# Optimization experiments

Hardware: AMD Instinct MI355X
Metric: run time of the kernel (lower is better)

Reference implementation:

```python
import jax, jax.numpy as jnp
import numpy as np

B, N, U = 8, 2048, 256
BN_EPS = 1e-3  # keras BatchNormalization default epsilon
ADJ_DENSITY = 0.008  # ~16 neighbors per node on average


def setup_inputs() -> dict:
    key = jax.random.key(0)
    ks = jax.random.split(key, 16)
    s = 0.05  # weight scale ('random_normal' init is small-stddev in keras)
    x = jax.random.normal(ks[0], (B, N, U), jnp.float32)
    # sparse binary adjacency stored dense (per-sample SpMM pattern)
    adj = (jax.random.uniform(ks[1], (B, N, N)) < ADJ_DENSITY).astype(jnp.float32)
    nodal_mask = jnp.ones((B, N), jnp.float32)
    return {
        'x': x, 'adj': adj, 'nodal_mask': nodal_mask,
        'W_lin': jax.random.normal(ks[2], (U, U)) * s, 'b_lin': jnp.zeros((U,)),
        'Wq_mp': jax.random.normal(ks[3], (3, U, U)) * s, 'bq_mp': jnp.zeros((3, U)),
        'Wk_mp': jax.random.normal(ks[4], (3, U, U)) * s, 'bk_mp': jnp.zeros((3, U)),
        'Wv_mp': jax.random.normal(ks[5], (3, U, U)) * s, 'bv_mp': jnp.zeros((3, U)),
        'Wk_att': jax.random.normal(ks[6], (U, U)) * s,
        'Wv_att': jax.random.normal(ks[7], (U, U)) * s,
        'Wq_att': jax.random.normal(ks[8], (U, U)) * s,
        'Wo_att': jax.random.normal(ks[9], (U, U)) * s,
        'bn_gamma': jnp.ones((U,)), 'bn_beta': jnp.zeros((U,)),
        'bn_mean': jnp.zeros((U,)), 'bn_var': jnp.ones((U,)),
        'W_proj': jax.random.normal(ks[10], (U, U)) * s, 'b_proj': jnp.zeros((U,)),
        'W_res': jax.random.normal(ks[11], (U, U)) * s, 'b_res': jnp.zeros((U,)),
    }


def _dympn(x, adj, Ws, bs, mask):
    # 3 message-passing layers, each applied K_l=2 times (inference value)
    for i in range(3):
        for _ in range(2):
            xn = jnp.einsum('bmn,bnd->bmd', adj, x)  # batched SpMM (graph_conv mode)
            x = jax.nn.silu(jnp.einsum('bmd,de->bme', xn, Ws[i]) + bs[i])
    return x * mask[:, :, None]


def reference(x, adj, nodal_mask, W_lin, b_lin, Wq_mp, bq_mp, Wk_mp, bk_mp,
              Wv_mp, bv_mp, Wk_att, Wv_att, Wq_att, Wo_att,
              bn_gamma, bn_beta, bn_mean, bn_var, W_proj, b_proj, W_res, b_res):
    initial_x = x
    adj = jax.lax.stop_gradient(adj)
    h = jnp.einsum('bnd,de->bne', x, W_lin) + b_lin
    q = _dympn(h, adj, Wq_mp, bq_mp, nodal_mask)
    k = _dympn(h, adj, Wk_mp, bk_mp, nodal_mask)
    v = _dympn(h, adj, Wv_mp, bv_mp, nodal_mask)
    # linear attention
    m = nodal_mask[:, :, None]
    pk = jax.nn.silu(jnp.einsum('bnd,de->bne', k, Wk_att) * m)
    pv = jnp.einsum('bnd,de->bne', v, Wv_att) * m
    pq = jnp.einsum('bnd,de->bne', q, Wq_att)
    kv = jnp.einsum('bnd,bne->bde', pk, pv)       # [B,U,U]
    attn = jnp.einsum('bnd,bde->bne', pq, kv)
    attn = jnp.einsum('bnd,de->bne', attn, Wo_att)
    # batch norm (inference: moving stats) over last axis
    y = attn + initial_x
    y = bn_gamma * (y - bn_mean) * jax.lax.rsqrt(bn_var + BN_EPS) + bn_beta
    out = jax.nn.silu(jnp.einsum('bnd,de->bne', y, W_proj) + b_proj)
    out = out + jnp.einsum('bnd,de->bne', initial_x, W_res) + b_res
    out = out * nodal_mask[:, :, None]
    return out
```

## Files before the change

kernel.cpp:

```cpp
#include <hip/hip_runtime.h>
#include <stdint.h>

#define NB 8
#define NN 2048
#define NU 256
#define CAP 64
#define BNEPS 0.001f
#define GSTR ((size_t)(NN * NU + 256))

typedef __attribute__((ext_vector_type(8))) short short8;
typedef __attribute__((ext_vector_type(4))) float floatx4;
typedef unsigned short u16;
typedef unsigned int u32;

__device__ __forceinline__ float bf2f(u16 u) {
  union { u32 i; float f; } c; c.i = ((u32)u) << 16; return c.f;
}
__device__ __forceinline__ u16 f2bf(float f) {
  union { float f; u32 i; } c; c.f = f;
  return (u16)((c.i + 0x7fffu + ((c.i >> 16) & 1u)) >> 16);
}
__device__ __forceinline__ void splitbf(float a, u16& h, u16& l) {
  h = f2bf(a);
  l = f2bf(a - bf2f(h));
}

enum : unsigned {
  F_BIAS = 2u, F_SILU = 4u, F_MASKPRE = 8u, F_MASKPOST = 16u,
  F_ADDX = 32u, F_BN = 64u, F_ADDT = 128u, F_BPERMAT = 512u,
  F_TPLANES = 1024u, F_OUTHL = 2048u, F_GSTRIDE = 8192u
};

#define TP_MAT 524288
#define TP_LO  4194304
#define MSZ ((size_t)NN * NU)

struct WPtrs { const float* p[16]; };

__global__ __launch_bounds__(256) void prologue_k(
    WPtrs wp, u16* __restrict__ wdst,
    const float* __restrict__ x, u16* __restrict__ xdst, size_t xLo,
    const float* __restrict__ adj, int* __restrict__ cnt, int* __restrict__ idx,
    float* __restrict__ ga, float* __restrict__ gb)
{
  int bid = blockIdx.x;
  int tid = threadIdx.x;
  __shared__ int c0;
  if (bid < 512) {
    int gid = bid * 256 + tid;
    int mat = gid >> 13;
    int rem = gid & 8191;
    int kb = rem >> 10;
    int n = (rem >> 2) & 255;
    int slot = rem & 3;
    int qv = (slot - (n >> 1)) & 3;
    int k0 = kb * 32 + qv * 8;
    const float* W = wp.p[mat];
    u32 oh[4], ol[4];
#pragma unroll
    for (int t2 = 0; t2 < 4; t2++) {
      float f0 = W[(size_t)(k0 + 2 * t2) * 256 + n];
      float f1 = W[(size_t)(k0 + 2 * t2 + 1) * 256 + n];
      u16 h0, l0, h1, l1;
      splitbf(f0, h0, l0);
      splitbf(f1, h1, l1);
      oh[t2] = (u32)h0 | ((u32)h1 << 16);
      ol[t2] = (u32)l0 | ((u32)l1 << 16);
    }
    uint4 qh; qh.x = oh[0]; qh.y = oh[1]; qh.z = oh[2]; qh.w = oh[3];
    uint4 ql; ql.x = ol[0]; ql.y = ol[1]; ql.z = ol[2]; ql.w = ol[3];
    *(uint4*)(wdst + (size_t)gid * 8) = qh;
    *(uint4*)(wdst + 1048576 + (size_t)gid * 8) = ql;
  } else if (bid < 4608) {
    size_t i = ((size_t)(bid - 512) * 256 + tid) * 4;
    float4 v = *(const float4*)(x + i);
    u16 h0, l0, h1, l1, h2, l2, h3, l3;
    splitbf(v.x, h0, l0); splitbf(v.y, h1, l1);
    splitbf(v.z, h2, l2); splitbf(v.w, h3, l3);
    uint2 H; H.x = (u32)h0 | ((u32)h1 << 16); H.y = (u32)h2 | ((u32)h3 << 16);
    uint2 L; L.x = (u32)l0 | ((u32)l1 << 16); L.y = (u32)l2 | ((u32)l3 << 16);
    *(uint2*)(xdst + i) = H;
    *(uint2*)(xdst + xLo + i) = L;
  } else if (bid < 20992) {
    int row = bid - 4608;
    const float* base = adj + (size_t)row * NN;
    if (tid == 0) c0 = 0;
    __syncthreads();
#pragma unroll
    for (int j = 0; j < 8; j++) {
      int n = j * 256 + tid;
      if (base[n] != 0.f) {
        int p = atomicAdd(&c0, 1);
        if (p < CAP) idx[(size_t)row * CAP + p] = n;
      }
    }
    __syncthreads();
    int cc = (c0 < CAP ? c0 : CAP);
    for (int p = cc + tid; p < CAP; p += 256) idx[(size_t)row * CAP + p] = -1;
    if (tid == 0) cnt[row] = cc;
  } else {
    int g = bid - 20992;
    float* base = (g < 24 ? ga : gb) + (size_t)(g % 24) * GSTR;
    base[tid] = 0.f;
  }
}

template <unsigned F>
__device__ __forceinline__ void gemm_epi(
    floatx4 (&acc)[2][2], int b, int bm, int w, int m16, int q,
    const float* __restrict__ bias, const float* __restrict__ mask,
    const float* __restrict__ xf32,
    const float* __restrict__ gma, const float* __restrict__ bta,
    const float* __restrict__ bmu, const float* __restrict__ bvr,
    const float* __restrict__ addt, void* __restrict__ outp, size_t oLo)
{
#pragma unroll
  for (int mt = 0; mt < 2; mt++) {
    if (F & F_TPLANES) {
      u16* oh = (u16*)outp + (size_t)b * TP_MAT;
      u16* ol = oh + TP_LO;
      int gr0 = bm + mt * 16 + q * 4;
#pragma unroll
      for (int nt = 0; nt < 2; nt++) {
        int col = w * 32 + nt * 16 + m16;
        u16 hh[4], ll[4];
#pragma unroll
        for (int r = 0; r < 4; r++) {
          float t2 = acc[mt][nt][r];
          float mv = mask[b * NN + gr0 + r];
          if (F & F_MASKPRE) t2 *= mv;
          if (F & F_SILU) t2 = t2 / (1.f + __expf(-t2));
          if (F & F_MASKPOST) t2 *= mv;
          splitbf(t2, hh[r], ll[r]);
        }
        uint2 H2, L2v;
        H2.x = (u32)hh[0] | ((u32)hh[1] << 16);
        H2.y = (u32)hh[2] | ((u32)hh[3] << 16);
        L2v.x = (u32)ll[0] | ((u32)ll[1] << 16);
        L2v.y = (u32)ll[2] | ((u32)ll[3] << 16);
        *(uint2*)(oh + (size_t)col * 2048 + gr0) = H2;
        *(uint2*)(ol + (size_t)col * 2048 + gr0) = L2v;
      }
    } else {
#pragma unroll
      for (int r = 0; r < 4; r++) {
        int gr = bm + mt * 16 + q * 4 + r;
        float mval = 1.f;
        if (F & (F_MASKPRE | F_MASKPOST)) mval = mask[b * NN + gr];
#pragma unroll
        for (int nt = 0; nt < 2; nt++) {
          int col = w * 32 + nt * 16 + m16;
          float t2 = acc[mt][nt][r];
          if (F & F_BIAS) t2 += bias[col];
          if (F & F_MASKPRE) t2 *= mval;
          if (F & F_SILU) t2 = t2 / (1.f + __expf(-t2));
          if (F & F_ADDX) t2 += xf32[((size_t)b * NN + gr) * NU + col];
          if (F & F_BN) t2 = gma[col] * (t2 - bmu[col]) * rsqrtf(bvr[col] + BNEPS) + bta[col];
          if (F & F_ADDT) t2 += addt[((size_t)b * NN + gr) * NU + col];
          if (F & F_MASKPOST) t2 *= mval;
          size_t o;
          if (F & F_GSTRIDE) o = (size_t)b * GSTR + (size_t)gr * NU + col;
          else o = ((size_t)b * NN + gr) * NU + col;
          if (F & F_OUTHL) {
            u16 h0, l0;
            splitbf(t2, h0, l0);
            ((u16*)outp)[o] = h0;
            ((u16*)outp)[o + oLo] = l0;
          } else {
            ((float*)outp)[o] = t2;
          }
        }
      }
    }
  }
}

#define LDSPAD_U16 28672

template <int NG, unsigned SF, unsigned F0, unsigned F1, unsigned F2, bool DK = false>
__global__ __launch_bounds__(512, 8) void gemm_k(
    const u16* __restrict__ A0, const u16* __restrict__ A1, const u16* __restrict__ A2,
    size_t aLo,
    const u16* __restrict__ W0, const u16* __restrict__ W1, const u16* __restrict__ W2,
    size_t wLo,
    const float* __restrict__ b0, const float* __restrict__ b1, const float* __restrict__ b2,
    const float* __restrict__ mask,
    const float* __restrict__ xf32,
    const float* __restrict__ gma, const float* __restrict__ bta,
    const float* __restrict__ bmu, const float* __restrict__ bvr,
    const float* __restrict__ addt,
    void* __restrict__ o0, void* __restrict__ o1, void* __restrict__ o2,
    size_t oLo,
    const float* __restrict__ gsrc,
    const float* __restrict__ sb0, const float* __restrict__ sb1, const float* __restrict__ sb2,
    const int* __restrict__ ncnt, const int* __restrict__ nidx)
{
  const int tid = threadIdx.x;
  const int id = blockIdx.x;
  const int xcd = id & 7;
  const int t = id >> 3;
  const int chain = (NG == 1) ? 0 : (t >> 6);
  const int xt = (NG == 1) ? t : (t & 63);
  const int b = xcd;
  const int bm = xt * 32;

  __shared__ alignas(16) u16 AB[LDSPAD_U16];
  u16* const Ah = AB;
  u16* const Al = AB + 32 * 264;

  const u16* Wsel = (chain == 0) ? W0 : (chain == 1 ? W1 : W2);
  if (F0 & F_BPERMAT) Wsel = W0 + (size_t)b * 65536;
  const u16* Whi = Wsel;
  const u16* Wlo = Whi + wLo;

  const int lane = tid & 63;
  const int w = tid >> 6;

  if constexpr (SF != 0u) {
    const float* __restrict__ gm = gsrc + (size_t)(chain * 8 + b) * GSTR + 256;
    const float* sb = (chain == 0) ? sb0 : (chain == 1 ? sb1 : sb2);
    const int c = lane * 4;
    float4 bb = *(const float4*)(sb + c);
    const int r0 = w * 4;
    int cnts[4];
    const int* ips[4];
    float4 av[4];
    int rowids[4];
#pragma unroll
    for (int i = 0; i < 4; i++) {
      rowids[i] = b * NN + bm + r0 + i;
      cnts[i] = ncnt[rowids[i]];
      ips[i] = nidx + (size_t)rowids[i] * CAP;
      av[i].x = av[i].y = av[i].z = av[i].w = 0.f;
    }
    int maxc = cnts[0];
    maxc = cnts[1] > maxc ? cnts[1] : maxc;
    maxc = cnts[2] > maxc ? cnts[2] : maxc;
    maxc = cnts[3] > maxc ? cnts[3] : maxc;
    for (int e = 0; e + 4 <= maxc; e += 4) {
#pragma unroll
      for (int i = 0; i < 4; i++) {
        if (e + 4 <= cnts[i]) {
          int4 i4 = *(const int4*)(ips[i] + e);
          float4 v0 = *(const float4*)(gm + ((size_t)i4.x << 8) + c);
          float4 v1 = *(const float4*)(gm + ((size_t)i4.y << 8) + c);
          float4 v2 = *(const float4*)(gm + ((size_t)i4.z << 8) + c);
          float4 v3 = *(const float4*)(gm + ((size_t)i4.w << 8) + c);
          av[i].x += v0.x + v1.x + v2.x + v3.x;
          av[i].y += v0.y + v1.y + v2.y + v3.y;
          av[i].z += v0.z + v1.z + v2.z + v3.z;
          av[i].w += v0.w + v1.w + v2.w + v3.w;
        }
      }
    }
#pragma unroll
    for (int i = 0; i < 4; i++) {
      for (int e = cnts[i] & ~3; e < cnts[i]; e++) {
        float4 v = *(const float4*)(gm + ((size_t)ips[i][e] << 8) + c);
        av[i].x += v.x; av[i].y += v.y; av[i].z += v.z; av[i].w += v.w;
      }
    }
#pragma unroll
    for (int i = 0; i < 4; i++) {
      float ov[4] = {av[i].x + bb.x, av[i].y + bb.y, av[i].z + bb.z, av[i].w + bb.w};
      float mv = (SF & F_MASKPOST) ? mask[rowids[i]] : 1.f;
      u16 hh[4], ll[4];
#pragma unroll
      for (int j = 0; j < 4; j++) {
        float t2 = ov[j];
        if (SF & F_SILU) t2 = t2 / (1.f + __expf(-t2));
        if (SF & F_MASKPOST) t2 *= mv;
        splitbf(t2, hh[j], ll[j]);
      }
      uint2 H; H.x = (u32)hh[0] | ((u32)hh[1] << 16); H.y = (u32)hh[2] | ((u32)hh[3] << 16);
      uint2 L; L.x = (u32)ll[0] | ((u32)ll[1] << 16); L.y = (u32)ll[2] | ((u32)ll[3] << 16);
      *(uint2*)&Ah[(r0 + i) * 264 + c] = H;
      *(uint2*)&Al[(r0 + i) * 264 + c] = L;
    }
  } else {
    const u16* Abase = (chain == 0) ? A0 : (chain == 1 ? A1 : A2);
    const u16* Ahp = Abase + (size_t)b * MSZ;
    const u16* Alp = Ahp + aLo;
    {
      int s = tid;
      int r = s >> 4;
      int c = (s & 15) << 4;
      size_t ao = (size_t)(bm + r) * 256 + c;
      *(uint4*)&Ah[r * 264 + c] = *(const uint4*)(Ahp + ao);
      *(uint4*)&Ah[r * 264 + c + 8] = *(const uint4*)(Ahp + ao + 8);
      *(uint4*)&Al[r * 264 + c] = *(const uint4*)(Alp + ao);
      *(uint4*)&Al[r * 264 + c + 8] = *(const uint4*)(Alp + ao + 8);
    }
  }
  __syncthreads();

  const int m16 = lane & 15;
  const int q = lane >> 4;

  floatx4 acc[2][2];
#pragma unroll
  for (int i = 0; i < 2; i++)
#pragma unroll
    for (int j = 0; j < 2; j++) acc[i][j] = (floatx4){0.f, 0.f, 0.f, 0.f};

#pragma unroll
  for (int kk = 0; kk < 8; kk++) {
    short8 bh[2], bl2[2];
#pragma unroll
    for (int nt = 0; nt < 2; nt++) {
      int n = w * 32 + nt * 16 + m16;
      size_t off = (size_t)kk * 8192 + (size_t)n * 32 + (size_t)(((q + (n >> 1)) & 3) * 8);
      bh[nt] = *(const short8*)(Whi + off);
      bl2[nt] = *(const short8*)(Wlo + off);
    }
#pragma unroll
    for (int mt = 0; mt < 2; mt++) {
      int row = mt * 16 + m16;
      short8 ah = *(const short8*)&Ah[row * 264 + kk * 32 + q * 8];
      short8 al2 = *(const short8*)&Al[row * 264 + kk * 32 + q * 8];
#pragma unroll
      for (int nt = 0; nt < 2; nt++) {
        acc[mt][nt] = __builtin_amdgcn_mfma_f32_16x16x32_bf16(ah, bh[nt], acc[mt][nt], 0, 0, 0);
        acc[mt][nt] = __builtin_amdgcn_mfma_f32_16x16x32_bf16(al2, bh[nt], acc[mt][nt], 0, 0, 0);
        acc[mt][nt] = __builtin_amdgcn_mfma_f32_16x16x32_bf16(ah, bl2[nt], acc[mt][nt], 0, 0, 0);
      }
    }
  }

  if constexpr (DK) {
#pragma unroll
    for (int mt = 0; mt < 2; mt++)
#pragma unroll
      for (int nt = 0; nt < 2; nt++) {
        int col = w * 32 + nt * 16 + m16;
        float bp = b1[col];
#pragma unroll
        for (int r = 0; r < 4; r++) {
          float t2 = acc[mt][nt][r] + bp;
          acc[mt][nt][r] = t2 / (1.f + __expf(-t2));
        }
      }
    __syncthreads();
    {
      const u16* Ahp = A1 + (size_t)b * MSZ;
      const u16* Alp = Ahp + aLo;
      int s = tid;
      int r = s >> 4;
      int c = (s & 15) << 4;
      size_t ao = (size_t)(bm + r) * 256 + c;
      *(uint4*)&Ah[r * 264 + c] = *(const uint4*)(Ahp + ao);
      *(uint4*)&Ah[r * 264 + c + 8] = *(const uint4*)(Ahp + ao + 8);
      *(uint4*)&Al[r * 264 + c] = *(const uint4*)(Alp + ao);
      *(uint4*)&Al[r * 264 + c + 8] = *(const uint4*)(Alp + ao + 8);
    }
    __syncthreads();
    const u16* W1h = W1;
    const u16* W1l = W1 + wLo;
#pragma unroll
    for (int kk = 0; kk < 8; kk++) {
      short8 bh[2], bl2[2];
#pragma unroll
      for (int nt = 0; nt < 2; nt++) {
        int n = w * 32 + nt * 16 + m16;
        size_t off = (size_t)kk * 8192 + (size_t)n * 32 + (size_t)(((q + (n >> 1)) & 3) * 8);
        bh[nt] = *(const short8*)(W1h + off);
        bl2[nt] = *(const short8*)(W1l + off);
      }
#pragma unroll
      for (int mt = 0; mt < 2; mt++) {
        int row = mt * 16 + m16;
        short8 ah = *(const short8*)&Ah[row * 264 + kk * 32 + q * 8];
        short8 al2 = *(const short8*)&Al[row * 264 + kk * 32 + q * 8];
#pragma unroll
        for (int nt = 0; nt < 2; nt++) {
          acc[mt][nt] = __builtin_amdgcn_mfma_f32_16x16x32_bf16(ah, bh[nt], acc[mt][nt], 0, 0, 0);
          acc[mt][nt] = __builtin_amdgcn_mfma_f32_16x16x32_bf16(al2, bh[nt], acc[mt][nt], 0, 0, 0);
          acc[mt][nt] = __builtin_amdgcn_mfma_f32_16x16x32_bf16(ah, bl2[nt], acc[mt][nt], 0, 0, 0);
        }
      }
    }
  }

  if (NG == 1 || chain == 0)
    gemm_epi<F0>(acc, b, bm, w, m16, q, b0, mask, xf32, gma, bta, bmu, bvr, addt, o0, oLo);
  else if (chain == 1)
    gemm_epi<F1>(acc, b, bm, w, m16, q, b1, mask, xf32, gma, bta, bmu, bvr, addt, o1, oLo);
  else
    gemm_epi<F2>(acc, b, bm, w, m16, q, b2, mask, xf32, gma, bta, bmu, bvr, addt, o2, oLo);
}

__global__ __launch_bounds__(256, 2) void kv_k(
    const u16* __restrict__ pkT, const u16* __restrict__ pvT, float* __restrict__ part)
{
  int et = blockIdx.x * 128;
  int dt = blockIdx.y * 128;
  int z = blockIdx.z;
  int b = z & 7;
  int p = z >> 3;
  int tid = threadIdx.x;
  int lane = tid & 63, w = tid >> 6;
  int m16 = lane & 15, q = lane >> 4;

  const u16* pkh = pkT + (size_t)b * TP_MAT;
  const u16* pkl = pkh + TP_LO;
  const u16* pvh = pvT + (size_t)b * TP_MAT;
  const u16* pvl = pvh + TP_LO;

  int d_base = dt + (w >> 1) * 64 + m16;
  int e_base = et + (w & 1) * 64 + m16;

  floatx4 acc[4][4];
#pragma unroll
  for (int i = 0; i < 4; i++)
#pragma unroll
    for (int j = 0; j < 4; j++) acc[i][j] = (floatx4){0.f, 0.f, 0.f, 0.f};

#pragma unroll
  for (int kt = 0; kt < 8; kt++) {
    int kc = p * 256 + kt * 32 + q * 8;
    short8 ah[4], al[4], bh[4], bl[4];
#pragma unroll
    for (int mt = 0; mt < 4; mt++) {
      size_t o = (size_t)(d_base + mt * 16) * 2048 + kc;
      ah[mt] = *(const short8*)(pkh + o);
      al[mt] = *(const short8*)(pkl + o);
    }
#pragma unroll
    for (int nt = 0; nt < 4; nt++) {
      size_t o = (size_t)(e_base + nt * 16) * 2048 + kc;
      bh[nt] = *(const short8*)(pvh + o);
      bl[nt] = *(const short8*)(pvl + o);
    }
#pragma unroll
    for (int mt = 0; mt < 4; mt++)
#pragma unroll
      for (int nt = 0; nt < 4; nt++) {
        acc[mt][nt] = __builtin_amdgcn_mfma_f32_16x16x32_bf16(ah[mt], bh[nt], acc[mt][nt], 0, 0, 0);
        acc[mt][nt] = __builtin_amdgcn_mfma_f32_16x16x32_bf16(al[mt], bh[nt], acc[mt][nt], 0, 0, 0);
        acc[mt][nt] = __builtin_amdgcn_mfma_f32_16x16x32_bf16(ah[mt], bl[nt], acc[mt][nt], 0, 0, 0);
      }
  }

#pragma unroll
  for (int mt = 0; mt < 4; mt++)
#pragma unroll
    for (int r = 0; r < 4; r++) {
      int d = dt + (w >> 1) * 64 + mt * 16 + q * 4 + r;
#pragma unroll
      for (int nt = 0; nt < 4; nt++) {
        int e = et + (w & 1) * 64 + nt * 16 + m16;
        part[(size_t)z * 65536 + (size_t)d * 256 + e] = acc[mt][nt][r];
      }
    }
}

__global__ __launch_bounds__(256) void kv_conv_k(const float* __restrict__ part, u16* __restrict__ dst)
{
  int gid = blockIdx.x * 256 + threadIdx.x;
  int b = gid >> 13;
  int rem = gid & 8191;
  int kb = rem >> 10;
  int e = (rem >> 2) & 255;
  int slot = rem & 3;
  int qv = (slot - (e >> 1)) & 3;
  int d0 = kb * 32 + qv * 8;
  const float* src = part + (size_t)b * 65536 + (size_t)d0 * 256 + e;
  u32 oh[4], ol[4];
#pragma unroll
  for (int t2 = 0; t2 < 4; t2++) {
    float s0 = 0.f, s1 = 0.f;
#pragma unroll
    for (int pp = 0; pp < 8; pp++) {
      const float* sp = src + (size_t)pp * 524288 + t2 * 512;
      s0 += sp[0];
      s1 += sp[256];
    }
    u16 h0, l0, h1, l1;
    splitbf(s0, h0, l0);
    splitbf(s1, h1, l1);
    oh[t2] = (u32)h0 | ((u32)h1 << 16);
    ol[t2] = (u32)l0 | ((u32)l1 << 16);
  }
  uint4 qh; qh.x = oh[0]; qh.y = oh[1]; qh.z = oh[2]; qh.w = oh[3];
  uint4 ql; ql.x = ol[0]; ql.y = ol[1]; ql.z = ol[2]; ql.w = ol[3];
  *(uint4*)(dst + (size_t)gid * 8) = qh;
  *(uint4*)(dst + 524288 + (size_t)gid * 8) = ql;
}

extern "C" void kernel_launch(void* const* d_in, const int* in_sizes, int n_in,
                              void* d_out, int out_size, void* d_ws, size_t ws_size,
                              hipStream_t stream)
{
  const float* x = (const float*)d_in[0];
  const float* adj = (const float*)d_in[1];
  const float* mask = (const float*)d_in[2];
  const float* W_lin = (const float*)d_in[3];
  const float* b_lin = (const float*)d_in[4];
  const float* Wq_mp = (const float*)d_in[5];
  const float* bq_mp = (const float*)d_in[6];
  const float* Wk_mp = (const float*)d_in[7];
  const float* bk_mp = (const float*)d_in[8];
  const float* Wv_mp = (const float*)d_in[9];
  const float* bv_mp = (const float*)d_in[10];
  const float* Wk_att = (const float*)d_in[11];
  const float* Wv_att = (const float*)d_in[12];
  const float* Wq_att = (const float*)d_in[13];
  const float* Wo_att = (const float*)d_in[14];
  const float* bn_gamma = (const float*)d_in[15];
  const float* bn_beta = (const float*)d_in[16];
  const float* bn_mean = (const float*)d_in[17];
  const float* bn_var = (const float*)d_in[18];
  const float* W_proj = (const float*)d_in[19];
  const float* b_proj = (const float*)d_in[20];
  const float* W_res = (const float*)d_in[21];
  const float* b_res = (const float*)d_in[22];

  char* ws = (char*)d_ws;
  int* CNT    = (int*)(ws + 0);
  int* IDX    = (int*)(ws + (1ull << 20));
  u16* WSZ    = (u16*)(ws + (5ull << 20));
  u16* KVS    = (u16*)(ws + (9ull << 20));
  float* KVP  = (float*)(ws + (11ull << 20));
  u16* XHL    = (u16*)(ws + (27ull << 20));
  u16* HHL    = (u16*)(ws + (43ull << 20));
  float* GA   = (float*)(ws + (59ull << 20));
  float* GB   = (float*)(ws + (110ull << 20));
  u16* PKT    = (u16*)(ws + (161ull << 20));
  u16* PVT    = (u16*)(ws + (177ull << 20));
  u16* ATT    = (u16*)(ws + (193ull << 20));
  u16* YHL    = (u16*)(ws + (209ull << 20));
  u16* PQHL   = (u16*)(ws + (225ull << 20));

  const size_t WLO = 1048576;
  const size_t KLO = 524288;
  const size_t A8  = 8 * MSZ;
  const unsigned FG = F_GSTRIDE;

  WPtrs wp;
  wp.p[0] = W_lin;
  wp.p[1] = Wq_mp; wp.p[2] = Wq_mp + 65536; wp.p[3] = Wq_mp + 131072;
  wp.p[4] = Wk_mp; wp.p[5] = Wk_mp + 65536; wp.p[6] = Wk_mp + 131072;
  wp.p[7] = Wv_mp; wp.p[8] = Wv_mp + 65536; wp.p[9] = Wv_mp + 131072;
  wp.p[10] = Wk_att; wp.p[11] = Wv_att; wp.p[12] = Wq_att; wp.p[13] = Wo_att;
  wp.p[14] = W_proj; wp.p[15] = W_res;
  prologue_k<<<21040, 256, 0, stream>>>(wp, WSZ, x, XHL, A8, adj, CNT, IDX, GA, GB);

  gemm_k<1, 0u, F_BIAS | F_OUTHL, 0u, 0u><<<512, 512, 0, stream>>>(
      XHL, XHL, XHL, A8, WSZ, WSZ, WSZ, WLO,
      b_lin, nullptr, nullptr, mask, nullptr,
      bn_gamma, bn_beta, bn_mean, bn_var, nullptr,
      HHL, nullptr, nullptr, A8,
      nullptr, nullptr, nullptr, nullptr, CNT, IDX);

  gemm_k<3, 0u, FG, FG, FG><<<1536, 512, 0, stream>>>(
      HHL, HHL, HHL, A8,
      WSZ + (size_t)1 * 65536, WSZ + (size_t)4 * 65536, WSZ + (size_t)7 * 65536, WLO,
      nullptr, nullptr, nullptr, mask, nullptr,
      bn_gamma, bn_beta, bn_mean, bn_var, nullptr,
      GA + 256, GA + 8 * GSTR + 256, GA + 16 * GSTR + 256, 0,
      nullptr, nullptr, nullptr, nullptr, CNT, IDX);

  for (int s = 1; s < 6; s++) {
    int iw = s >> 1;
    int ib = (s - 1) >> 1;
    float* Gin = (s & 1) ? GA : GB;
    float* Gout = (s & 1) ? GB : GA;
    gemm_k<3, F_BIAS | F_SILU, FG, FG, FG><<<1536, 512, 0, stream>>>(
        nullptr, nullptr, nullptr, 0,
        WSZ + (size_t)(1 + iw) * 65536, WSZ + (size_t)(4 + iw) * 65536,
        WSZ + (size_t)(7 + iw) * 65536, WLO,
        nullptr, nullptr, nullptr, mask, nullptr,
        bn_gamma, bn_beta, bn_mean, bn_var, nullptr,
        Gout + 256, Gout + 8 * GSTR + 256, Gout + 16 * GSTR + 256, 0,
        Gin, bq_mp + ib * 256, bk_mp + ib * 256, bv_mp + ib * 256, CNT, IDX);
  }

  gemm_k<3, F_BIAS | F_SILU | F_MASKPOST,
         F_OUTHL, F_SILU | F_MASKPRE | F_TPLANES, F_MASKPOST | F_TPLANES>
      <<<1536, 512, 0, stream>>>(
      nullptr, nullptr, nullptr, 0,
      WSZ + (size_t)12 * 65536, WSZ + (size_t)10 * 65536, WSZ + (size_t)11 * 65536, WLO,
      nullptr, nullptr, nullptr, mask, nullptr,
      bn_gamma, bn_beta, bn_mean, bn_var, nullptr,
      PQHL, PKT, PVT, A8,
      GB, bq_mp + 512, bk_mp + 512, bv_mp + 512, CNT, IDX);

  kv_k<<<dim3(2, 2, 64), 256, 0, stream>>>(PKT, PVT, KVP);
  kv_conv_k<<<256, 256, 0, stream>>>(KVP, KVS);

  gemm_k<1, 0u, F_BPERMAT | F_OUTHL, 0u, 0u><<<512, 512, 0, stream>>>(
      PQHL, PQHL, PQHL, A8, KVS, KVS, KVS, KLO,
      nullptr, nullptr, nullptr, mask, nullptr,
      bn_gamma, bn_beta, bn_mean, bn_var, nullptr,
      ATT, nullptr, nullptr, A8,
      nullptr, nullptr, nullptr, nullptr, CNT, IDX);

  gemm_k<1, 0u, F_ADDX | F_BN | F_OUTHL, 0u, 0u><<<512, 512, 0, stream>>>(
      ATT, ATT, ATT, A8,
      WSZ + (size_t)13 * 65536, nullptr, nullptr, WLO,
      nullptr, nullptr, nullptr, mask, x,
      bn_gamma, bn_beta, bn_mean, bn_var, nullptr,
      YHL, nullptr, nullptr, A8,
      nullptr, nullptr, nullptr, nullptr, CNT, IDX);

  gemm_k<1, 0u, F_BIAS | F_MASKPOST, 0u, 0u, true><<<512, 512, 0, stream>>>(
      YHL, XHL, YHL, A8,
      WSZ + (size_t)14 * 65536, WSZ + (size_t)15 * 65536, nullptr, WLO,
      b_res, b_proj, nullptr, mask, nullptr,
      bn_gamma, bn_beta, bn_mean, bn_var, nullptr,
      d_out, nullptr, nullptr, 0,
      nullptr, nullptr, nullptr, nullptr, CNT, IDX);

  (void)in_sizes; (void)n_in; (void)out_size; (void)ws_size;
}
```

Before: 762.3 us.

## Fold W_lin into first MP weights and Wo_att into KV matrix

Precomputes W_lin·W_mp[0] and b_lin·W_mp[0] in the prologue, so the first message-passing GEMM reads x directly and the separate h = x·W_lin GEMM goes away. It also folds Wo_att into the per-batch KV matrix (KV·Wo) with a small kernel, merging the attention GEMM and the output-projection GEMM into one pass with BN and residual. This removes two full B×N×U GEMM launches and their intermediate traffic, at the cost of a few small weight-product kernels and reassociated rounding.

```diff
diff --git a/kernel.cpp b/kernel.cpp
--- a/kernel.cpp
+++ b/kernel.cpp
@@ -34,6 +34,7 @@
 #define TP_MAT 524288
 #define TP_LO  4194304
 #define MSZ ((size_t)NN * NU)
+#define WFLO 196608
 
 struct WPtrs { const float* p[16]; };
 
@@ -41,11 +42,13 @@
     WPtrs wp, u16* __restrict__ wdst,
     const float* __restrict__ x, u16* __restrict__ xdst, size_t xLo,
     const float* __restrict__ adj, int* __restrict__ cnt, int* __restrict__ idx,
-    float* __restrict__ ga, float* __restrict__ gb)
+    float* __restrict__ ga, float* __restrict__ gb,
+    const float* __restrict__ blin, float* __restrict__ wf, float* __restrict__ bf)
 {
   int bid = blockIdx.x;
   int tid = threadIdx.x;
   __shared__ int c0;
+  __shared__ float arow[256];
   if (bid < 512) {
     int gid = bid * 256 + tid;
     int mat = gid >> 13;
@@ -98,11 +101,60 @@
     int cc = (c0 < CAP ? c0 : CAP);
     for (int p = cc + tid; p < CAP; p += 256) idx[(size_t)row * CAP + p] = -1;
     if (tid == 0) cnt[row] = cc;
-  } else {
+  } else if (bid < 21040) {
     int g = bid - 20992;
     float* base = (g < 24 ? ga : gb) + (size_t)(g % 24) * GSTR;
     base[tid] = 0.f;
-  }
+  } else {
+    int idx2 = bid - 21040;
+    if (idx2 < 768) {
+      int c = idx2 >> 8;
+      int r = idx2 & 255;
+      const float* Wc = wp.p[1 + 3 * c];
+      arow[tid] = wp.p[0][r * 256 + tid];
+      __syncthreads();
+      float acc = 0.f;
+      for (int k = 0; k < 256; k++) acc += arow[k] * Wc[k * 256 + tid];
+      wf[(size_t)c * 65536 + (size_t)r * 256 + tid] = acc;
+    } else {
+      int c = idx2 - 768;
+      const float* Wc = wp.p[1 + 3 * c];
+      arow[tid] = blin[tid];
+      __syncthreads();
+      float acc = 0.f;
+      for (int k = 0; k < 256; k++) acc += arow[k] * Wc[k * 256 + tid];
+      bf[c * 256 + tid] = acc;
+    }
+  }
+}
+
+__global__ __launch_bounds__(256) void convf_k(
+    const float* __restrict__ wf, u16* __restrict__ wfz)
+{
+  int gid = blockIdx.x * 256 + threadIdx.x;
+  int m = gid >> 13;
+  int rem = gid & 8191;
+  int kb = rem >> 10;
+  int n = (rem >> 2) & 255;
+  int slot = rem & 3;
+  int qv = (slot - (n >> 1)) & 3;
+  int k0 = kb * 32 + qv * 8;
+  const float* W = wf + (size_t)m * 65536;
+  u32 oh[4], ol[4];
+#pragma unroll
+  for (int t2 = 0; t2 < 4; t2++) {
+    float f0 = W[(size_t)(k0 + 2 * t2) * 256 + n];
+    float f1 = W[(size_t)(k0 + 2 * t2 + 1) * 256 + n];
+    u16 h0, l0, h1, l1;
+    splitbf(f0, h0, l0);
+    splitbf(f1, h1, l1);
+    oh[t2] = (u32)h0 | ((u32)h1 << 16);
+    ol[t2] = (u32)l0 | ((u32)l1 << 16);
+  }
+  uint4 qh; qh.x = oh[0]; qh.y = oh[1]; qh.z = oh[2]; qh.w = oh[3];
+  uint4 ql; ql.x = ol[0]; ql.y = ol[1]; ql.z = ol[2]; ql.w = ol[3];
+  *(uint4*)(wfz + (size_t)gid * 8) = qh;
+  *(uint4*)(wfz + WFLO + (size_t)gid * 8) = ql;
 }
 
 template <unsigned F>
@@ -175,8 +227,6 @@
   }
 }
 
-#define LDSPAD_U16 28672
-
 template <int NG, unsigned SF, unsigned F0, unsigned F1, unsigned F2, bool DK = false>
 __global__ __launch_bounds__(512, 8) void gemm_k(
     const u16* __restrict__ A0, const u16* __restrict__ A1, const u16* __restrict__ A2,
@@ -204,9 +254,8 @@
   const int b = xcd;
   const int bm = xt * 32;
 
-  __shared__ alignas(16) u16 AB[LDSPAD_U16];
-  u16* const Ah = AB;
-  u16* const Al = AB + 32 * 264;
+  __shared__ alignas(16) u16 Ah[32 * 264];
+  __shared__ alignas(16) u16 Al[32 * 264];
 
   const u16* Wsel = (chain == 0) ? W0 : (chain == 1 ? W1 : W2);
   if (F0 & F_BPERMAT) Wsel = W0 + (size_t)b * 65536;
@@ -454,7 +503,28 @@
     }
 }
 
-__global__ __launch_bounds__(256) void kv_conv_k(const float* __restrict__ part, u16* __restrict__ dst)
+__global__ __launch_bounds__(256) void kvo_k(
+    const float* __restrict__ part, const float* __restrict__ Wo,
+    float* __restrict__ kvo)
+{
+  __shared__ float krow[256];
+  int bid = blockIdx.x;
+  int b = bid >> 8;
+  int d = bid & 255;
+  int tid = threadIdx.x;
+  float s = 0.f;
+  size_t base = (size_t)b * 65536 + (size_t)d * 256 + tid;
+#pragma unroll
+  for (int pp = 0; pp < 8; pp++) s += part[base + (size_t)pp * 524288];
+  krow[tid] = s;
+  __syncthreads();
+  float acc = 0.f;
+  for (int e = 0; e < 256; e++) acc += krow[e] * Wo[(size_t)e * 256 + tid];
+  kvo[(size_t)b * 65536 + (size_t)d * 256 + tid] = acc;
+}
+
+__global__ __launch_bounds__(256) void kvoconv_k(
+    const float* __restrict__ kvo, u16* __restrict__ dst)
 {
   int gid = blockIdx.x * 256 + threadIdx.x;
   int b = gid >> 13;
@@ -464,17 +534,12 @@
   int slot = rem & 3;
   int qv = (slot - (e >> 1)) & 3;
   int d0 = kb * 32 + qv * 8;
-  const float* src = part + (size_t)b * 65536 + (size_t)d0 * 256 + e;
+  const float* src = kvo + (size_t)b * 65536 + (size_t)d0 * 256 + e;
   u32 oh[4], ol[4];
 #pragma unroll
   for (int t2 = 0; t2 < 4; t2++) {
-    float s0 = 0.f, s1 = 0.f;
-#pragma unroll
-    for (int pp = 0; pp < 8; pp++) {
-      const float* sp = src + (size_t)pp * 524288 + t2 * 512;
-      s0 += sp[0];
-      s1 += sp[256];
-    }
+    float s0 = src[t2 * 512];
+    float s1 = src[t2 * 512 + 256];
     u16 h0, l0, h1, l1;
     splitbf(s0, h0, l0);
     splitbf(s1, h1, l1);
@@ -522,12 +587,14 @@
   u16* KVS    = (u16*)(ws + (9ull << 20));
   float* KVP  = (float*)(ws + (11ull << 20));
   u16* XHL    = (u16*)(ws + (27ull << 20));
-  u16* HHL    = (u16*)(ws + (43ull << 20));
+  float* WF   = (float*)(ws + (43ull << 20));
+  float* BF   = (float*)(ws + (44ull << 20));
+  float* KVO  = (float*)(ws + (45ull << 20));
+  u16* WFZ    = (u16*)(ws + (48ull << 20));
   float* GA   = (float*)(ws + (59ull << 20));
   float* GB   = (float*)(ws + (110ull << 20));
   u16* PKT    = (u16*)(ws + (161ull << 20));
   u16* PVT    = (u16*)(ws + (177ull << 20));
-  u16* ATT    = (u16*)(ws + (193ull << 20));
   u16* YHL    = (u16*)(ws + (209ull << 20));
   u16* PQHL   = (u16*)(ws + (225ull << 20));
 
@@ -543,19 +610,14 @@
   wp.p[7] = Wv_mp; wp.p[8] = Wv_mp + 65536; wp.p[9] = Wv_mp + 131072;
   wp.p[10] = Wk_att; wp.p[11] = Wv_att; wp.p[12] = Wq_att; wp.p[13] = Wo_att;
   wp.p[14] = W_proj; wp.p[15] = W_res;
-  prologue_k<<<21040, 256, 0, stream>>>(wp, WSZ, x, XHL, A8, adj, CNT, IDX, GA, GB);
-
-  gemm_k<1, 0u, F_BIAS | F_OUTHL, 0u, 0u><<<512, 512, 0, stream>>>(
-      XHL, XHL, XHL, A8, WSZ, WSZ, WSZ, WLO,
-      b_lin, nullptr, nullptr, mask, nullptr,
-      bn_gamma, bn_beta, bn_mean, bn_var, nullptr,
-      HHL, nullptr, nullptr, A8,
-      nullptr, nullptr, nullptr, nullptr, CNT, IDX);
-
-  gemm_k<3, 0u, FG, FG, FG><<<1536, 512, 0, stream>>>(
-      HHL, HHL, HHL, A8,
-      WSZ + (size_t)1 * 65536, WSZ + (size_t)4 * 65536, WSZ + (size_t)7 * 65536, WLO,
-      nullptr, nullptr, nullptr, mask, nullptr,
+  prologue_k<<<21811, 256, 0, stream>>>(wp, WSZ, x, XHL, A8, adj, CNT, IDX,
+                                        GA, GB, b_lin, WF, BF);
+  convf_k<<<96, 256, 0, stream>>>(WF, WFZ);
+
+  gemm_k<3, 0u, FG | F_BIAS, FG | F_BIAS, FG | F_BIAS><<<1536, 512, 0, stream>>>(
+      XHL, XHL, XHL, A8,
+      WFZ, WFZ + 65536, WFZ + 131072, WFLO,
+      BF, BF + 256, BF + 512, mask, nullptr,
       bn_gamma, bn_beta, bn_mean, bn_var, nullptr,
       GA + 256, GA + 8 * GSTR + 256, GA + 16 * GSTR + 256, 0,
       nullptr, nullptr, nullptr, nullptr, CNT, IDX);
@@ -586,18 +648,11 @@
       GB, bq_mp + 512, bk_mp + 512, bv_mp + 512, CNT, IDX);
 
   kv_k<<<dim3(2, 2, 64), 256, 0, stream>>>(PKT, PVT, KVP);
-  kv_conv_k<<<256, 256, 0, stream>>>(KVP, KVS);
-
-  gemm_k<1, 0u, F_BPERMAT | F_OUTHL, 0u, 0u><<<512, 512, 0, stream>>>(
+  kvo_k<<<2048, 256, 0, stream>>>(KVP, Wo_att, KVO);
+  kvoconv_k<<<256, 256, 0, stream>>>(KVO, KVS);
+
+  gemm_k<1, 0u, F_BPERMAT | F_ADDX | F_BN | F_OUTHL, 0u, 0u><<<512, 512, 0, stream>>>(
       PQHL, PQHL, PQHL, A8, KVS, KVS, KVS, KLO,
-      nullptr, nullptr, nullptr, mask, nullptr,
-      bn_gamma, bn_beta, bn_mean, bn_var, nullptr,
-      ATT, nullptr, nullptr, A8,
-      nullptr, nullptr, nullptr, nullptr, CNT, IDX);
-
-  gemm_k<1, 0u, F_ADDX | F_BN | F_OUTHL, 0u, 0u><<<512, 512, 0, stream>>>(
-      ATT, ATT, ATT, A8,
-      WSZ + (size_t)13 * 65536, nullptr, nullptr, WLO,
       nullptr, nullptr, nullptr, mask, x,
       bn_gamma, bn_beta, bn_mean, bn_var, nullptr,
       YHL, nullptr, nullptr, A8,
```

Result: faster. 739.4 us (-3.0%).
